# Performance work log

Hardware: AMD Instinct MI355X
Metric: run time of the kernel (lower is better)

The kernel has to match this reference:

```python
import jax, jax.numpy as jnp
import numpy as np

TEMP = 0.05
DIAG_PENALTY = 1e12
EPS = 1e-8  # matches torch F.cosine_similarity eps


def setup_inputs() -> dict:
    key = jax.random.key(0)
    x = jax.random.normal(key, (8192, 768), dtype=jnp.float32)
    return {"x": x}


def reference(x):
    n = x.shape[0]
    # labels: swap adjacent pairs -> i - (i%2)*2 + 1  (i.e. i XOR 1)
    idx = jnp.arange(n)
    labels = idx - (idx % 2) * 2 + 1
    # cosine similarity matrix via normalize + GEMM (same math as broadcasted
    # F.cosine_similarity: dot(x_i, x_j) / (max(||x_i||,eps) * max(||x_j||,eps)))
    norms = jnp.maximum(jnp.linalg.norm(x, axis=-1, keepdims=True), EPS)
    xn = x / norms
    sim = xn @ xn.T                                   # [N, N]
    sim = sim - jnp.eye(n, dtype=sim.dtype) * DIAG_PENALTY
    logits = sim / TEMP
    # mean cross-entropy with stable log-softmax
    logp = jax.nn.log_softmax(logits, axis=-1)
    loss = -jnp.mean(jnp.take_along_axis(logp, labels[:, None], axis=-1))
    return loss
```

## Files before the change

kernel.cpp:

```cpp
#include <hip/hip_runtime.h>
#include <hip/hip_bf16.h>

#define N 8192
#define D 768
#define TEMP_INV 20.0f
#define NTILES 2080

typedef __attribute__((ext_vector_type(4))) float f32x4;
typedef __attribute__((ext_vector_type(4))) int i32x4;
typedef __attribute__((ext_vector_type(8))) int i32x8;

#define SCALE1 0x7F7F7F7F


__global__ __launch_bounds__(256) void norm_kernel(
    const float* __restrict__ x, unsigned char* __restrict__ xn,
    float* __restrict__ rowsum) {
  int t = threadIdx.x, w = t >> 6, lane = t & 63;
  int row = blockIdx.x * 4 + w;
  const float4* xr = (const float4*)(x + (size_t)row * D);
  float4 v[3];
  v[0] = xr[lane];
  v[1] = xr[lane + 64];
  v[2] = xr[lane + 128];
  float ss = 0.0f;
#pragma unroll
  for (int i = 0; i < 3; ++i)
    ss += v[i].x * v[i].x + v[i].y * v[i].y + v[i].z * v[i].z + v[i].w * v[i].w;
#pragma unroll
  for (int m = 32; m; m >>= 1) ss += __shfl_xor(ss, m);
  float inv = 1.0f / fmaxf(sqrtf(ss), 1e-8f);
  unsigned int* xo = (unsigned int*)(xn + (size_t)row * D);
#pragma unroll
  for (int i = 0; i < 3; ++i) {
    int p = __builtin_amdgcn_cvt_pk_fp8_f32(v[i].x * inv, v[i].y * inv, 0, false);
    p = __builtin_amdgcn_cvt_pk_fp8_f32(v[i].z * inv, v[i].w * inv, p, true);
    xo[lane + 64 * i] = p;
  }
  if (t < 4) rowsum[blockIdx.x * 4 + t] = 0.0f;
}

__global__ __launch_bounds__(256, 2) void sim_kernel(
    const unsigned char* __restrict__ xn, float* __restrict__ rowsum,
    float* __restrict__ pos) {
  static const short stbase[37] = {
      0, 36, 100, 164, 228, 292, 356, 420,
      484, 520, 584, 648, 712, 776, 840,
      904, 940, 1004, 1068, 1132, 1196,
      1260, 1296, 1360, 1424, 1488,
      1552, 1588, 1652, 1716,
      1780, 1816, 1880,
      1944, 1980,
      2044, 2080};
  static const char sti[36] = {0,0,0,0,0,0,0,0, 1,1,1,1,1,1,1, 2,2,2,2,2,2,
                               3,3,3,3,3, 4,4,4,4, 5,5,5, 6,6, 7};
  static const char stj[36] = {0,1,2,3,4,5,6,7, 1,2,3,4,5,6,7, 2,3,4,5,6,7,
                               3,4,5,6,7, 4,5,6,7, 5,6,7, 6,7, 7};
  int b = blockIdx.x;
  int p = 260 * (b & 7) + (b >> 3);
  int s = 0;
  while ((int)stbase[s + 1] <= p) ++s;
  int wofs = p - stbase[s];
  int SI = sti[s], SJ = stj[s];
  int bi, bj;
  if (SI == SJ) {
    int di = 0, cum = 0;
    while (wofs >= cum + (8 - di)) { cum += 8 - di; ++di; }
    bi = SI * 8 + di;
    bj = SI * 8 + di + (wofs - cum);
  } else {
    bi = SI * 8 + (wofs >> 3);
    bj = SJ * 8 + (wofs & 7);
  }

  __shared__ i32x4 As4[2][128 * 8];
  __shared__ i32x4 Bs4[2][128 * 8];

  int t = threadIdx.x;
  int w = t >> 6, lane = t & 63;
  int q = lane >> 4, cl = lane & 15;
  int wm = w >> 1, wn = w & 1;

  f32x4 acc[4][4] = {};

  int ulog = (((t & 7) ^ ((t >> 3) & 7))) * 16;
  const unsigned char* Ab = xn + (size_t)(bi * 128 + (t >> 3)) * D + ulog;
  const unsigned char* Bb = xn + (size_t)(bj * 128 + (t >> 3)) * D + ulog;

  int u0 = (2 * q) ^ (cl & 7);
  int u1 = u0 ^ 1;

  auto stage = [&](int buf, int k0) {
#pragma unroll
    for (int rr = 0; rr < 4; ++rr) {
      __builtin_amdgcn_global_load_lds(
          (const __attribute__((address_space(1))) unsigned int*)(Ab + (size_t)(rr * 32) * D + k0),
          (__attribute__((address_space(3))) unsigned int*)(&As4[buf][rr * 256 + t]), 16, 0, 0);
      __builtin_amdgcn_global_load_lds(
          (const __attribute__((address_space(1))) unsigned int*)(Bb + (size_t)(rr * 32) * D + k0),
          (__attribute__((address_space(3))) unsigned int*)(&Bs4[buf][rr * 256 + t]), 16, 0, 0);
    }
  };

  stage(0, 0);
  asm volatile("s_waitcnt vmcnt(0)" ::: "memory");
  __builtin_amdgcn_s_barrier();
  __builtin_amdgcn_sched_barrier(0);

#pragma unroll
  for (int kc = 0; kc < 6; ++kc) {
    const int cur = kc & 1;
    if (kc < 5) stage(cur ^ 1, (kc + 1) * 128);

    union Frag { i32x8 v8; struct { i32x4 lo, hi; } pr; };
    Frag a[4], bb[4];
#pragma unroll
    for (int m = 0; m < 4; ++m) {
      int rowb = (wm * 64 + m * 16 + cl) * 8;
      a[m].pr.lo = As4[cur][rowb + u0];
      a[m].pr.hi = As4[cur][rowb + u1];
    }
#pragma unroll
    for (int n = 0; n < 4; ++n) {
      int rowb = (wn * 64 + n * 16 + cl) * 8;
      bb[n].pr.lo = Bs4[cur][rowb + u0];
      bb[n].pr.hi = Bs4[cur][rowb + u1];
    }
#pragma unroll
    for (int m = 0; m < 4; ++m)
#pragma unroll
      for (int n = 0; n < 4; ++n)
        acc[m][n] = __builtin_amdgcn_mfma_scale_f32_16x16x128_f8f6f4(
            a[m].v8, bb[n].v8, acc[m][n], 0, 0, 0, SCALE1, 0, SCALE1);

    if (kc < 5) {
      asm volatile("s_waitcnt vmcnt(0)" ::: "memory");
      __builtin_amdgcn_s_barrier();
      __builtin_amdgcn_sched_barrier(0);
    }
  }

  int gi0 = bi * 128 + wm * 64;
  int gj0 = bj * 128 + wn * 64;

  float rowp[4][4] = {};
  float colp[4] = {};

  if (bi == bj) {
#pragma unroll
    for (int m = 0; m < 4; ++m)
#pragma unroll
      for (int n = 0; n < 4; ++n)
#pragma unroll
        for (int r = 0; r < 4; ++r) {
          float sv = acc[m][n][r];
          int row = gi0 + m * 16 + q * 4 + r;
          int col = gj0 + n * 16 + cl;
          float e = __expf(TEMP_INV * sv - 20.0f);
          if (col == row) e = 0.0f;
          if (col == (row ^ 1)) pos[row] = TEMP_INV * sv;
          rowp[m][r] += e;
        }
  } else {
#pragma unroll
    for (int m = 0; m < 4; ++m)
#pragma unroll
      for (int n = 0; n < 4; ++n)
#pragma unroll
        for (int r = 0; r < 4; ++r) {
          float e = __expf(TEMP_INV * acc[m][n][r] - 20.0f);
          rowp[m][r] += e;
          colp[n] += e;
        }
  }

#pragma unroll
  for (int m = 0; m < 4; ++m)
#pragma unroll
    for (int r = 0; r < 4; ++r) {
      float v = rowp[m][r];
      v += __shfl_xor(v, 1);
      v += __shfl_xor(v, 2);
      v += __shfl_xor(v, 4);
      v += __shfl_xor(v, 8);
      if (cl == 0) atomicAdd(&rowsum[gi0 + m * 16 + q * 4 + r], v);
    }
  if (bi != bj) {
#pragma unroll
    for (int n = 0; n < 4; ++n) {
      float v = colp[n];
      v += __shfl_xor(v, 16);
      v += __shfl_xor(v, 32);
      if (q == 0) atomicAdd(&rowsum[gj0 + n * 16 + cl], v);
    }
  }
}

__global__ __launch_bounds__(1024) void loss_kernel(
    const float* __restrict__ rowsum, const float* __restrict__ pos,
    float* __restrict__ out) {
  int t = threadIdx.x;
  const float4* r4 = (const float4*)rowsum;
  const float4* p4 = (const float4*)pos;
  float acc = 0.0f;
#pragma unroll
  for (int it = 0; it < 2; ++it) {
    int i = t + it * 1024;
    float4 r = r4[i], pp = p4[i];
    acc += 80.0f + __logf(r.x) + __logf(r.y) + __logf(r.z) + __logf(r.w)
           - pp.x - pp.y - pp.z - pp.w;
  }
#pragma unroll
  for (int m = 32; m; m >>= 1) acc += __shfl_xor(acc, m);
  __shared__ float wsum[16];
  if ((t & 63) == 0) wsum[t >> 6] = acc;
  __syncthreads();
  if (t == 0) {
    float tot = 0.0f;
#pragma unroll
    for (int i = 0; i < 16; ++i) tot += wsum[i];
    out[0] = tot / (float)N;
  }
}

extern "C" void kernel_launch(void* const* d_in, const int* in_sizes, int n_in,
                              void* d_out, int out_size, void* d_ws, size_t ws_size,
                              hipStream_t stream) {
  const float* x = (const float*)d_in[0];
  float* rowsum = (float*)d_ws;
  float* pos = rowsum + N;
  unsigned char* xn = (unsigned char*)(rowsum + 2 * N + 16);

  norm_kernel<<<N / 4, 256, 0, stream>>>(x, xn, rowsum);
  sim_kernel<<<NTILES, 256, 0, stream>>>(xn, rowsum, pos);
  loss_kernel<<<1, 1024, 0, stream>>>(rowsum, pos, (float*)d_out);
}
```

Before: 136.2 us.

## Enlarge sim tiles to 256x256 with 8 waves and phased LDS/MFMA interleave

```diff
diff --git a/kernel.cpp b/kernel.cpp
--- a/kernel.cpp
+++ b/kernel.cpp
@@ -4,7 +4,7 @@
 #define N 8192
 #define D 768
 #define TEMP_INV 20.0f
-#define NTILES 2080
+#define NTILES 528
 
 typedef __attribute__((ext_vector_type(4))) float f32x4;
 typedef __attribute__((ext_vector_type(4))) int i32x4;
@@ -40,24 +40,24 @@
   if (t < 4) rowsum[blockIdx.x * 4 + t] = 0.0f;
 }
 
-__global__ __launch_bounds__(256, 2) void sim_kernel(
+__global__ __launch_bounds__(512, 2) void sim_kernel(
     const unsigned char* __restrict__ xn, float* __restrict__ rowsum,
     float* __restrict__ pos) {
   static const short stbase[37] = {
-      0, 36, 100, 164, 228, 292, 356, 420,
-      484, 520, 584, 648, 712, 776, 840,
-      904, 940, 1004, 1068, 1132, 1196,
-      1260, 1296, 1360, 1424, 1488,
-      1552, 1588, 1652, 1716,
-      1780, 1816, 1880,
-      1944, 1980,
-      2044, 2080};
+      0, 10, 26, 42, 58, 74, 90, 106, 122,
+      132, 148, 164, 180, 196, 212, 228,
+      238, 254, 270, 286, 302, 318,
+      328, 344, 360, 376, 392,
+      402, 418, 434, 450,
+      460, 476, 492,
+      502, 518,
+      528};
   static const char sti[36] = {0,0,0,0,0,0,0,0, 1,1,1,1,1,1,1, 2,2,2,2,2,2,
                                3,3,3,3,3, 4,4,4,4, 5,5,5, 6,6, 7};
   static const char stj[36] = {0,1,2,3,4,5,6,7, 1,2,3,4,5,6,7, 2,3,4,5,6,7,
                                3,4,5,6,7, 4,5,6,7, 5,6,7, 6,7, 7};
   int b = blockIdx.x;
-  int p = 260 * (b & 7) + (b >> 3);
+  int p = 66 * (b & 7) + (b >> 3);
   int s = 0;
   while ((int)stbase[s + 1] <= p) ++s;
   int wofs = p - stbase[s];
@@ -65,74 +65,131 @@
   int bi, bj;
   if (SI == SJ) {
     int di = 0, cum = 0;
-    while (wofs >= cum + (8 - di)) { cum += 8 - di; ++di; }
-    bi = SI * 8 + di;
-    bj = SI * 8 + di + (wofs - cum);
+    while (wofs >= cum + (4 - di)) { cum += 4 - di; ++di; }
+    bi = SI * 4 + di;
+    bj = SI * 4 + di + (wofs - cum);
   } else {
-    bi = SI * 8 + (wofs >> 3);
-    bj = SJ * 8 + (wofs & 7);
-  }
-
-  __shared__ i32x4 As4[2][128 * 8];
-  __shared__ i32x4 Bs4[2][128 * 8];
+    bi = SI * 4 + (wofs >> 2);
+    bj = SJ * 4 + (wofs & 3);
+  }
+
+  __shared__ i32x4 As4[2][2048];
+  __shared__ i32x4 Bs4[2][2048];
 
   int t = threadIdx.x;
   int w = t >> 6, lane = t & 63;
   int q = lane >> 4, cl = lane & 15;
-  int wm = w >> 1, wn = w & 1;
-
-  f32x4 acc[4][4] = {};
+  int wm = w >> 2, wn = w & 3;
+
+  f32x4 acc[8][4] = {};
 
   int ulog = (((t & 7) ^ ((t >> 3) & 7))) * 16;
-  const unsigned char* Ab = xn + (size_t)(bi * 128 + (t >> 3)) * D + ulog;
-  const unsigned char* Bb = xn + (size_t)(bj * 128 + (t >> 3)) * D + ulog;
+  const unsigned char* Ab = xn + (size_t)(bi * 256 + (t >> 3)) * D + ulog;
+  const unsigned char* Bb = xn + (size_t)(bj * 256 + (t >> 3)) * D + ulog;
 
   int u0 = (2 * q) ^ (cl & 7);
   int u1 = u0 ^ 1;
 
-  auto stage = [&](int buf, int k0) {
-#pragma unroll
-    for (int rr = 0; rr < 4; ++rr) {
+  auto stageA = [&](int buf, int k0) {
+#pragma unroll
+    for (int rr = 0; rr < 4; ++rr)
       __builtin_amdgcn_global_load_lds(
-          (const __attribute__((address_space(1))) unsigned int*)(Ab + (size_t)(rr * 32) * D + k0),
-          (__attribute__((address_space(3))) unsigned int*)(&As4[buf][rr * 256 + t]), 16, 0, 0);
+          (const __attribute__((address_space(1))) unsigned int*)(Ab + (size_t)(rr * 64) * D + k0),
+          (__attribute__((address_space(3))) unsigned int*)(&As4[buf][rr * 512 + t]), 16, 0, 0);
+  };
+  auto stageB = [&](int buf, int k0) {
+#pragma unroll
+    for (int rr = 0; rr < 4; ++rr)
       __builtin_amdgcn_global_load_lds(
-          (const __attribute__((address_space(1))) unsigned int*)(Bb + (size_t)(rr * 32) * D + k0),
-          (__attribute__((address_space(3))) unsigned int*)(&Bs4[buf][rr * 256 + t]), 16, 0, 0);
-    }
+          (const __attribute__((address_space(1))) unsigned int*)(Bb + (size_t)(rr * 64) * D + k0),
+          (__attribute__((address_space(3))) unsigned int*)(&Bs4[buf][rr * 512 + t]), 16, 0, 0);
   };
 
-  stage(0, 0);
+  stageA(0, 0);
+  stageB(0, 0);
   asm volatile("s_waitcnt vmcnt(0)" ::: "memory");
   __builtin_amdgcn_s_barrier();
   __builtin_amdgcn_sched_barrier(0);
 
+  union Frag { i32x8 v8; struct { i32x4 lo, hi; } pr; };
+
 #pragma unroll
   for (int kc = 0; kc < 6; ++kc) {
     const int cur = kc & 1;
-    if (kc < 5) stage(cur ^ 1, (kc + 1) * 128);
-
-    union Frag { i32x8 v8; struct { i32x4 lo, hi; } pr; };
-    Frag a[4], bb[4];
-#pragma unroll
-    for (int m = 0; m < 4; ++m) {
-      int rowb = (wm * 64 + m * 16 + cl) * 8;
-      a[m].pr.lo = As4[cur][rowb + u0];
-      a[m].pr.hi = As4[cur][rowb + u1];
-    }
-#pragma unroll
-    for (int n = 0; n < 4; ++n) {
+    const int k1 = (kc + 1) * 128;
+    Frag a[4], a2[4], bb[2];
+
+#pragma unroll
+    for (int n = 0; n < 2; ++n) {
       int rowb = (wn * 64 + n * 16 + cl) * 8;
       bb[n].pr.lo = Bs4[cur][rowb + u0];
       bb[n].pr.hi = Bs4[cur][rowb + u1];
     }
 #pragma unroll
-    for (int m = 0; m < 4; ++m)
-#pragma unroll
-      for (int n = 0; n < 4; ++n)
+    for (int m = 0; m < 4; ++m) {
+      int rowb = (wm * 128 + m * 16 + cl) * 8;
+      a[m].pr.lo = As4[cur][rowb + u0];
+      a[m].pr.hi = As4[cur][rowb + u1];
+    }
+    if (kc < 5) stageA(cur ^ 1, k1);
+    __builtin_amdgcn_s_barrier();
+    asm volatile("s_waitcnt lgkmcnt(0)" ::: "memory");
+    __builtin_amdgcn_sched_barrier(0);
+    __builtin_amdgcn_s_setprio(1);
+#pragma unroll
+    for (int m = 0; m < 4; ++m)
+#pragma unroll
+      for (int n = 0; n < 2; ++n)
         acc[m][n] = __builtin_amdgcn_mfma_scale_f32_16x16x128_f8f6f4(
             a[m].v8, bb[n].v8, acc[m][n], 0, 0, 0, SCALE1, 0, SCALE1);
-
+    __builtin_amdgcn_s_setprio(0);
+    __builtin_amdgcn_s_barrier();
+    __builtin_amdgcn_sched_barrier(0);
+
+#pragma unroll
+    for (int m = 0; m < 4; ++m) {
+      int rowb = (wm * 128 + (m + 4) * 16 + cl) * 8;
+      a2[m].pr.lo = As4[cur][rowb + u0];
+      a2[m].pr.hi = As4[cur][rowb + u1];
+    }
+    if (kc < 5) stageB(cur ^ 1, k1);
+    __builtin_amdgcn_s_barrier();
+    asm volatile("s_waitcnt lgkmcnt(0)" ::: "memory");
+    __builtin_amdgcn_sched_barrier(0);
+    __builtin_amdgcn_s_setprio(1);
+#pragma unroll
+    for (int m = 0; m < 4; ++m)
+#pragma unroll
+      for (int n = 0; n < 2; ++n)
+        acc[m + 4][n] = __builtin_amdgcn_mfma_scale_f32_16x16x128_f8f6f4(
+            a2[m].v8, bb[n].v8, acc[m + 4][n], 0, 0, 0, SCALE1, 0, SCALE1);
+    __builtin_amdgcn_s_setprio(0);
+    __builtin_amdgcn_s_barrier();
+    __builtin_amdgcn_sched_barrier(0);
+
+#pragma unroll
+    for (int n = 0; n < 2; ++n) {
+      int rowb = (wn * 64 + (n + 2) * 16 + cl) * 8;
+      bb[n].pr.lo = Bs4[cur][rowb + u0];
+      bb[n].pr.hi = Bs4[cur][rowb + u1];
+    }
+    __builtin_amdgcn_s_barrier();
+    asm volatile("s_waitcnt lgkmcnt(0)" ::: "memory");
+    __builtin_amdgcn_sched_barrier(0);
+    __builtin_amdgcn_s_setprio(1);
+#pragma unroll
+    for (int m = 0; m < 4; ++m)
+#pragma unroll
+      for (int n = 0; n < 2; ++n)
+        acc[m][n + 2] = __builtin_amdgcn_mfma_scale_f32_16x16x128_f8f6f4(
+            a[m].v8, bb[n].v8, acc[m][n + 2], 0, 0, 0, SCALE1, 0, SCALE1);
+#pragma unroll
+    for (int m = 0; m < 4; ++m)
+#pragma unroll
+      for (int n = 0; n < 2; ++n)
+        acc[m + 4][n + 2] = __builtin_amdgcn_mfma_scale_f32_16x16x128_f8f6f4(
+            a2[m].v8, bb[n].v8, acc[m + 4][n + 2], 0, 0, 0, SCALE1, 0, SCALE1);
+    __builtin_amdgcn_s_setprio(0);
     if (kc < 5) {
       asm volatile("s_waitcnt vmcnt(0)" ::: "memory");
       __builtin_amdgcn_s_barrier();
@@ -140,15 +197,15 @@
     }
   }
 
-  int gi0 = bi * 128 + wm * 64;
-  int gj0 = bj * 128 + wn * 64;
-
-  float rowp[4][4] = {};
+  int gi0 = bi * 256 + wm * 128;
+  int gj0 = bj * 256 + wn * 64;
+
+  float rowp[8][4] = {};
   float colp[4] = {};
 
   if (bi == bj) {
 #pragma unroll
-    for (int m = 0; m < 4; ++m)
+    for (int m = 0; m < 8; ++m)
 #pragma unroll
       for (int n = 0; n < 4; ++n)
 #pragma unroll
@@ -163,7 +220,7 @@
         }
   } else {
 #pragma unroll
-    for (int m = 0; m < 4; ++m)
+    for (int m = 0; m < 8; ++m)
 #pragma unroll
       for (int n = 0; n < 4; ++n)
 #pragma unroll
@@ -175,7 +232,7 @@
   }
 
 #pragma unroll
-  for (int m = 0; m < 4; ++m)
+  for (int m = 0; m < 8; ++m)
 #pragma unroll
     for (int r = 0; r < 4; ++r) {
       float v = rowp[m][r];
@@ -232,6 +289,6 @@
   unsigned char* xn = (unsigned char*)(rowsum + 2 * N + 16);
 
   norm_kernel<<<N / 4, 256, 0, stream>>>(x, xn, rowsum);
-  sim_kernel<<<NTILES, 256, 0, stream>>>(xn, rowsum, pos);
+  sim_kernel<<<NTILES, 512, 0, stream>>>(xn, rowsum, pos);
   loss_kernel<<<1, 1024, 0, stream>>>(rowsum, pos, (float*)d_out);
 }
```

Result: slower. 151.7 us (+11.4%).
